# Kernel optimization log

Measured on AMD Instinct MI355X. Metric: run time of the kernel, lower is better.

## Reference

```python
import jax, jax.numpy as jnp
import numpy as np

R = 8192   # rows of the input matrix (attention sequence dim)
F = 4096   # total input feature columns
L = 2048   # number of gathered columns (len(in_keys))


def setup_inputs() -> dict:
    key = jax.random.key(0)
    k1, k2, k3 = jax.random.split(key, 3)
    inputs = jax.random.normal(k1, (R, F), dtype=jnp.float32)
    in_idxs = jax.random.randint(k2, (L,), 0, F)
    weights = jax.random.normal(k3, (L, 3), dtype=jnp.float32)
    return {"inputs": inputs, "in_idxs": in_idxs, "weights": weights}


def reference(inputs, in_idxs, weights):
    # gather: torch.index_select(inputs, 1, in_idxs) -> [R, L]
    sel = jnp.take(inputs, in_idxs, axis=1)
    # QKV projection: [R, L] @ [L, 3] -> [R, 3]; chunk -> q, k, v each [R, 1]
    qkv = sel @ weights
    q, k, v = qkv[:, 0:1], qkv[:, 1:2], qkv[:, 2:3]
    d_k = q.shape[-1]  # = 1
    # scaled dot-product attention over the row dim: logits [R, R]
    logits = (q @ k.T) / jnp.sqrt(jnp.float32(d_k))
    attn = jax.nn.softmax(logits, axis=-1)
    values = attn @ v  # [R, 1]
    # out = activation(values[-1:, ]) -> [1, 1]
    return jax.nn.sigmoid(values[-1:, :])
```

## Files before the change

### kernel.cpp

```cpp
#include <hip/hip_runtime.h>
#include <math.h>

#define RR 8192
#define FF 4096
#define LL 2048
#define NBLK 1024
#define TPB 512

#define WS_W1  0
#define WS_W2  FF
#define WS_Q   (2 * FF)
#define WS_P   (2 * FF + 16)

__global__ __launch_bounds__(1024) void prep(const float* __restrict__ in,
                                             const int* __restrict__ idx,
                                             const float* __restrict__ wts,
                                             float* __restrict__ ws) {
    __shared__ float wsh[FF];
    __shared__ float qred[16];

    const int t = threadIdx.x, lane = t & 63, wv = t >> 6;
    const int b = blockIdx.x;

    for (int i = t; i < FF; i += 1024) wsh[i] = 0.f;
    __syncthreads();

    if (b == 0) {
        const float* lastrow = in + (size_t)(RR - 1) * FF;
        float qp = 0.f;
#pragma unroll
        for (int l = t; l < LL; l += 1024) {
            const int c = idx[l];
            qp += lastrow[c] * wts[3 * l + 0];
            atomicAdd(&wsh[c], wts[3 * l + 1]);
        }
        for (int o = 32; o > 0; o >>= 1) qp += __shfl_down(qp, o);
        if (lane == 0) qred[wv] = qp;
        __syncthreads();
        if (t < FF / 4)
            *(float4*)(ws + WS_W1 + t * 4) = *(const float4*)&wsh[t * 4];
        if (t == 0) {
            float q = 0.f;
#pragma unroll
            for (int i = 0; i < 16; ++i) q += qred[i];
            ws[WS_Q] = q;
        }
    } else {
#pragma unroll
        for (int l = t; l < LL; l += 1024) {
            atomicAdd(&wsh[idx[l]], wts[3 * l + 2]);
        }
        __syncthreads();
        if (t < FF / 4)
            *(float4*)(ws + WS_W2 + t * 4) = *(const float4*)&wsh[t * 4];
    }
}

__global__ __launch_bounds__(TPB, 8) void gemv_kv(const float* __restrict__ in,
                                                  const float* __restrict__ ws,
                                                  float* __restrict__ partials) {
    __shared__ float w1s[FF];
    __shared__ float w2s[FF];
    __shared__ float kv[8][2];

    const int t = threadIdx.x, lane = t & 63, wv = t >> 6;
    const int row = blockIdx.x * 8 + wv;
    const float* __restrict__ x = in + (size_t)row * FF;

    const float q = ws[WS_Q];

    const float4* __restrict__ wsrc1 = (const float4*)(ws + WS_W1);
    const float4* __restrict__ wsrc2 = (const float4*)(ws + WS_W2);
    const float4 s10 = wsrc1[t], s11 = wsrc1[512 + t];
    const float4 s20 = wsrc2[t], s21 = wsrc2[512 + t];

    float k = 0.f, v = 0.f;
#pragma unroll
    for (int i = 0; i < 4; ++i) {
        const int c = i * 256 + lane * 4;
        const float4 xv = *(const float4*)(x + c);
        const float4 a1 = *(const float4*)(ws + WS_W1 + c);
        const float4 a2 = *(const float4*)(ws + WS_W2 + c);
        k += xv.x * a1.x + xv.y * a1.y + xv.z * a1.z + xv.w * a1.w;
        v += xv.x * a2.x + xv.y * a2.y + xv.z * a2.z + xv.w * a2.w;
    }

    ((float4*)w1s)[t] = s10; ((float4*)w1s)[512 + t] = s11;
    ((float4*)w2s)[t] = s20; ((float4*)w2s)[512 + t] = s21;
    __syncthreads();

#pragma unroll
    for (int i = 4; i < 16; ++i) {
        const int c = i * 256 + lane * 4;
        const float4 xv = *(const float4*)(x + c);
        const float4 a1 = *(const float4*)&w1s[c];
        const float4 a2 = *(const float4*)&w2s[c];
        k += xv.x * a1.x + xv.y * a1.y + xv.z * a1.z + xv.w * a1.w;
        v += xv.x * a2.x + xv.y * a2.y + xv.z * a2.z + xv.w * a2.w;
    }
    for (int o = 32; o > 0; o >>= 1) { k += __shfl_down(k, o); v += __shfl_down(v, o); }
    if (lane == 0) { kv[wv][0] = k; kv[wv][1] = v; }
    __syncthreads();

    if (t == 0) {
        float m = -INFINITY;
#pragma unroll
        for (int r = 0; r < 8; ++r) m = fmaxf(m, q * kv[r][0]);
        float se = 0.f, sv = 0.f;
#pragma unroll
        for (int r = 0; r < 8; ++r) {
            const float e = expf(q * kv[r][0] - m);
            se += e;
            sv += e * kv[r][1];
        }
        partials[blockIdx.x * 3 + 0] = m;
        partials[blockIdx.x * 3 + 1] = se;
        partials[blockIdx.x * 3 + 2] = sv;
    }
}

__global__ __launch_bounds__(TPB) void combine(const float* __restrict__ partials,
                                               float* __restrict__ out) {
    const int t = threadIdx.x, lane = t & 63, wv = t >> 6;
    float lm[2], lse[2], lsv[2];
    float m = -INFINITY;
#pragma unroll
    for (int i = 0; i < 2; ++i) {
        const int b = t + i * TPB;
        lm[i]  = partials[b * 3 + 0];
        lse[i] = partials[b * 3 + 1];
        lsv[i] = partials[b * 3 + 2];
        m = fmaxf(m, lm[i]);
    }

    __shared__ float red[8], red2[8], red3[8], bc[1];
    for (int o = 32; o > 0; o >>= 1) m = fmaxf(m, __shfl_down(m, o));
    if (lane == 0) red[wv] = m;
    __syncthreads();
    if (t == 0) {
        float x = red[0];
#pragma unroll
        for (int i = 1; i < 8; ++i) x = fmaxf(x, red[i]);
        bc[0] = x;
    }
    __syncthreads();
    const float gm = bc[0];

    float se = 0.f, sv = 0.f;
#pragma unroll
    for (int i = 0; i < 2; ++i) {
        const float s = expf(lm[i] - gm);
        se += lse[i] * s;
        sv += lsv[i] * s;
    }
    for (int o = 32; o > 0; o >>= 1) { se += __shfl_down(se, o); sv += __shfl_down(sv, o); }
    if (lane == 0) { red2[wv] = se; red3[wv] = sv; }
    __syncthreads();
    if (t == 0) {
        float S = 0.f, V = 0.f;
#pragma unroll
        for (int i = 0; i < 8; ++i) { S += red2[i]; V += red3[i]; }
        out[0] = 1.0f / (1.0f + expf(-(V / S)));
    }
}

extern "C" void kernel_launch(void* const* d_in, const int* in_sizes, int n_in,
                              void* d_out, int out_size, void* d_ws, size_t ws_size,
                              hipStream_t stream) {
    const float* inputs = (const float*)d_in[0];
    const int*   idx    = (const int*)d_in[1];
    const float* wts    = (const float*)d_in[2];
    float* out = (float*)d_out;
    float* ws  = (float*)d_ws;

    prep<<<2, 1024, 0, stream>>>(inputs, idx, wts, ws);
    gemv_kv<<<NBLK, TPB, 0, stream>>>(inputs, ws, ws + WS_P);
    combine<<<1, TPB, 0, stream>>>(ws + WS_P, out);
}
```

Measured before the change: 34.28 us.

## Fuse softmax combine into GEMV kernel via per-block completion flags

The separate combine kernel is removed. Each GEMV block publishes its partial max, sum and weighted-value triple, then release-stores a magic flag. Block 0 spins on all 1024 flags and performs the final log-sum-exp merge and sigmoid itself. The prep kernel clears the flags. This removes one kernel launch and its inter-kernel gap, at the cost of a spin-wait in block 0 that depends on every other block making progress.

```diff
diff --git a/kernel.cpp b/kernel.cpp
--- a/kernel.cpp
+++ b/kernel.cpp
@@ -6,11 +6,13 @@
 #define LL 2048
 #define NBLK 1024
 #define TPB 512
+#define MAGIC 0x13571357u
 
 #define WS_W1  0
 #define WS_W2  FF
 #define WS_Q   (2 * FF)
 #define WS_P   (2 * FF + 16)
+#define WS_F   (WS_P + 3 * NBLK)
 
 __global__ __launch_bounds__(1024) void prep(const float* __restrict__ in,
                                              const int* __restrict__ idx,
@@ -53,21 +55,25 @@
         __syncthreads();
         if (t < FF / 4)
             *(float4*)(ws + WS_W2 + t * 4) = *(const float4*)&wsh[t * 4];
+        ((unsigned int*)(ws + WS_F))[t] = 0u;
     }
 }
 
-__global__ __launch_bounds__(TPB, 8) void gemv_kv(const float* __restrict__ in,
-                                                  const float* __restrict__ ws,
-                                                  float* __restrict__ partials) {
+__global__ __launch_bounds__(TPB, 8) void gemv_combine(const float* __restrict__ in,
+                                                       float* __restrict__ ws,
+                                                       float* __restrict__ out) {
     __shared__ float w1s[FF];
     __shared__ float w2s[FF];
     __shared__ float kv[8][2];
+    __shared__ float red[8], red2[8], red3[8], bc[1];
 
     const int t = threadIdx.x, lane = t & 63, wv = t >> 6;
     const int row = blockIdx.x * 8 + wv;
     const float* __restrict__ x = in + (size_t)row * FF;
+    const float q = ws[WS_Q];
 
-    const float q = ws[WS_Q];
+    unsigned int* const flags = (unsigned int*)(ws + WS_F);
+    float* const partials = ws + WS_P;
 
     const float4* __restrict__ wsrc1 = (const float4*)(ws + WS_W1);
     const float4* __restrict__ wsrc2 = (const float4*)(ws + WS_W2);
@@ -113,35 +119,37 @@
             se += e;
             sv += e * kv[r][1];
         }
-        partials[blockIdx.x * 3 + 0] = m;
-        partials[blockIdx.x * 3 + 1] = se;
-        partials[blockIdx.x * 3 + 2] = sv;
+        float* p = partials + blockIdx.x * 3;
+        p[0] = m; p[1] = se; p[2] = sv;
+        __hip_atomic_store(flags + blockIdx.x, MAGIC, __ATOMIC_RELEASE, __HIP_MEMORY_SCOPE_AGENT);
     }
-}
+    if (blockIdx.x != 0) return;
 
-__global__ __launch_bounds__(TPB) void combine(const float* __restrict__ partials,
-                                               float* __restrict__ out) {
-    const int t = threadIdx.x, lane = t & 63, wv = t >> 6;
+    while (__hip_atomic_load(flags + t, __ATOMIC_RELAXED, __HIP_MEMORY_SCOPE_AGENT) != MAGIC) {}
+    while (__hip_atomic_load(flags + t + TPB, __ATOMIC_RELAXED, __HIP_MEMORY_SCOPE_AGENT) != MAGIC) {}
+    __syncthreads();
+    if (t == 0)
+        (void)__hip_atomic_load(flags, __ATOMIC_ACQUIRE, __HIP_MEMORY_SCOPE_AGENT);
+    __syncthreads();
+
     float lm[2], lse[2], lsv[2];
     float m = -INFINITY;
 #pragma unroll
     for (int i = 0; i < 2; ++i) {
-        const int b = t + i * TPB;
-        lm[i]  = partials[b * 3 + 0];
-        lse[i] = partials[b * 3 + 1];
-        lsv[i] = partials[b * 3 + 2];
+        const int p = t + i * TPB;
+        lm[i]  = partials[p * 3 + 0];
+        lse[i] = partials[p * 3 + 1];
+        lsv[i] = partials[p * 3 + 2];
         m = fmaxf(m, lm[i]);
     }
-
-    __shared__ float red[8], red2[8], red3[8], bc[1];
     for (int o = 32; o > 0; o >>= 1) m = fmaxf(m, __shfl_down(m, o));
     if (lane == 0) red[wv] = m;
     __syncthreads();
     if (t == 0) {
-        float x = red[0];
+        float xx = red[0];
 #pragma unroll
-        for (int i = 1; i < 8; ++i) x = fmaxf(x, red[i]);
-        bc[0] = x;
+        for (int i = 1; i < 8; ++i) xx = fmaxf(xx, red[i]);
+        bc[0] = xx;
     }
     __syncthreads();
     const float gm = bc[0];
@@ -174,6 +182,5 @@
     float* ws  = (float*)d_ws;
 
     prep<<<2, 1024, 0, stream>>>(inputs, idx, wts, ws);
-    gemv_kv<<<NBLK, TPB, 0, stream>>>(inputs, ws, ws + WS_P);
-    combine<<<1, TPB, 0, stream>>>(ws + WS_P, out);
+    gemv_combine<<<NBLK, TPB, 0, stream>>>(inputs, ws, out);
 }
```

Result: slower. 59.18 us (+72.6%).
